# Kernel tuning notes

Measured on AMD Instinct MI355X. Metric: run time of the kernel, lower is better.

## Reference

```python
import jax, jax.numpy as jnp
import numpy as np
from jax import lax

N_BITS = 4  # init kwarg n_bits
Q_SCALE = 2.0 ** (N_BITS - 1) - 1.0  # signed n-bit levels


def ste_round(x):
    # straight-through rounding (identity gradient)
    return x + lax.stop_gradient(jnp.round(x) - x)


def quant_signed(x):
    # clip to [-1,1], quantize to 2^(n-1)-1 signed levels with STE
    return ste_round(jnp.clip(x, -1.0, 1.0) * Q_SCALE) / Q_SCALE


def qconv(x, w):
    # QuantizeConv: 3x3 stride-1 pad-1 conv with n-bit quantized weights
    return lax.conv_general_dilated(x, quant_signed(w), window_strides=(1, 1),
                                    padding=((1, 1), (1, 1)),
                                    dimension_numbers=('NCHW', 'OIHW', 'NCHW'))


def qact_conv(x, g, b):
    # QuantizeSignedActSBN (conv): per-channel scale/bias then signed quant
    return quant_signed(x * g[None, :, None, None] + b[None, :, None, None])


def qact_fc(x, g, b):
    return quant_signed(x * g[None, :] + b[None, :])


def maxpool2(x):
    return lax.reduce_window(x, -jnp.inf, lax.max, (1, 1, 2, 2), (1, 1, 2, 2), 'VALID')


def setup_inputs() -> dict:
    key = jax.random.key(0)
    ks = jax.random.split(key, 32)
    B = 512
    x = jax.random.normal(ks[0], (B, 3, 32, 32), dtype=jnp.float32)
    chans = [(64, 3), (64, 64), (128, 64), (128, 128), (256, 128), (256, 256)]
    inp = {'x': x}
    ki = 1
    for i, (co, ci) in enumerate(chans, start=1):
        inp[f'w{i}'] = jax.random.normal(ks[ki], (co, ci, 3, 3), dtype=jnp.float32) * 0.05; ki += 1
        inp[f'g{i}'] = jax.random.uniform(ks[ki], (co,), dtype=jnp.float32, minval=0.5, maxval=1.5); ki += 1
        inp[f'b{i}'] = jax.random.normal(ks[ki], (co,), dtype=jnp.float32) * 0.05; ki += 1
    # FC head: 4096 -> 512 -> 10 (torch Linear weight layout [out, in])
    inp['wf1'] = jax.random.normal(ks[ki], (512, 4096), dtype=jnp.float32) * 0.02; ki += 1
    inp['gf1'] = jax.random.uniform(ks[ki], (512,), dtype=jnp.float32, minval=0.5, maxval=1.5); ki += 1
    inp['bf1'] = jax.random.normal(ks[ki], (512,), dtype=jnp.float32) * 0.05; ki += 1
    inp['wf2'] = jax.random.normal(ks[ki], (10, 512), dtype=jnp.float32) * 0.05; ki += 1
    inp['gf2'] = jax.random.uniform(ks[ki], (10,), dtype=jnp.float32, minval=0.5, maxval=1.5); ki += 1
    inp['bf2'] = jax.random.normal(ks[ki], (10,), dtype=jnp.float32) * 0.05; ki += 1
    return inp


def reference(x, w1, g1, b1, w2, g2, b2, w3, g3, b3, w4, g4, b4, w5, g5, b5, w6, g6, b6,
              wf1, gf1, bf1, wf2, gf2, bf2):
    h = jax.nn.relu(qact_conv(qconv(x, w1), g1, b1))
    h = jax.nn.relu(qact_conv(qconv(h, w2), g2, b2))
    h = maxpool2(h)  # 32 -> 16
    h = jax.nn.relu(qact_conv(qconv(h, w3), g3, b3))
    h = jax.nn.relu(qact_conv(qconv(h, w4), g4, b4))
    h = maxpool2(h)  # 16 -> 8
    h = jax.nn.relu(qact_conv(qconv(h, w5), g5, b5))
    h = jax.nn.relu(qact_conv(qconv(h, w6), g6, b6))
    h = maxpool2(h)  # 8 -> 4 => 256*4*4 = 4096
    h = h.reshape(h.shape[0], -1)
    h = jax.nn.relu(qact_fc(h @ quant_signed(wf1).T, gf1, bf1))
    h = qact_fc(h @ quant_signed(wf2).T, gf2, bf2)
    return h
```

## Files before the change

### kernel.cpp

```cpp
#include <hip/hip_runtime.h>


typedef __attribute__((ext_vector_type(4))) int v4i;

#if defined(__has_builtin)
# if __has_builtin(__builtin_amdgcn_sdot4)
#  define HAS_SDOT4 1
# endif
#endif

__device__ __forceinline__ int dot4_i8(int a, int b, int c) {
#ifdef HAS_SDOT4
    return __builtin_amdgcn_sdot4(a, b, c, false);
#else
    c += ((a      ) & 0xff) * (int)(signed char)(b      );
    c += ((a >>  8) & 0xff) * (int)(signed char)(b >>  8);
    c += ((a >> 16) & 0xff) * (int)(signed char)(b >> 16);
    c += ((a >> 24) & 0xff) * (int)(signed char)(b >> 24);
    return c;
#endif
}

__device__ __forceinline__ void gld_lds16(const void* g, void* l) {
    __builtin_amdgcn_global_load_lds(
        (const __attribute__((address_space(1))) unsigned int*)g,
        (__attribute__((address_space(3))) unsigned int*)l, 16, 0, 0);
}

#define O_QW1    0u
#define O_QWF2   4096u
#define O_ZERO   10240u
#define O_QWT2   16384u
#define O_QWT3   65536u
#define O_QWT4   147456u
#define O_QWT5   294912u
#define O_QWT6   589824u
#define O_QWF1   1179648u
#define O_BUFA   3276800u
#define O_BUFB   36831232u

__device__ __forceinline__ signed char quant_w(double v) {
    return (signed char)(int)rint(fmin(fmax(v, -1.0), 1.0) * 7.0);
}

__device__ __forceinline__ void quantw_body(const float* __restrict__ w,
                                            signed char* __restrict__ q, int i, int n) {
    if (i < n) q[i] = quant_w((double)w[i]);
}

__device__ __forceinline__ void quantw_t8p_body(const float* __restrict__ w,
                                                signed char* __restrict__ o,
                                                int CI, int i, int n) {
    if (i < n) {
        const int b  = i & 15;
        const int t  = i >> 4;
        const int rows_per_grp = CI * 36;
        const int grp  = t / rows_per_grp;
        int rr = t - grp * rows_per_grp;
        const int pass = rr / 2304;
        rr -= pass * 2304;
        const int c    = rr / 576;
        const int row  = rr - c * 576;
        const int co_l = row / 9;
        const int tap  = row - co_l * 9;
        const int co = grp * 64 + co_l;
        const int ci = pass * 64 + c * 16 + b;
        o[i] = quant_w((double)w[(co * CI + ci) * 9 + tap]);
    }
}

__device__ __forceinline__ void quantw_fc1_body(const float* __restrict__ w,
                                                signed char* __restrict__ o, int i) {
    if (i < 512 * 4096) {
        int j  = i >> 12;
        int kn = i & 4095;
        int px = kn >> 8;
        int c  = kn & 255;
        int ko = c * 16 + px;
        o[i] = quant_w((double)w[j * 4096 + ko]);
    }
}

__global__ __launch_bounds__(256) void prep_k(
    const float* __restrict__ w1,  signed char* __restrict__ qw1,
    const float* __restrict__ wf2, signed char* __restrict__ qwf2,
    const float* __restrict__ w2,  signed char* __restrict__ qwt2,
    const float* __restrict__ w3,  signed char* __restrict__ qwt3,
    const float* __restrict__ w4,  signed char* __restrict__ qwt4,
    const float* __restrict__ w5,  signed char* __restrict__ qwt5,
    const float* __restrict__ w6,  signed char* __restrict__ qwt6,
    const float* __restrict__ wf1, signed char* __restrict__ qwf1,
    unsigned char* __restrict__ zs)
{
    const int blk = blockIdx.x;
    const int t   = threadIdx.x;
    if (blk == 0 && t < 16) ((int4*)zs)[t] = int4{0, 0, 0, 0};
    if      (blk < 7)    quantw_body(w1, qw1, blk * 256 + t, 1728);
    else if (blk < 27)   quantw_body(wf2, qwf2, (blk - 7) * 256 + t, 5120);
    else if (blk < 171)  quantw_t8p_body(w2, qwt2, 64,  (blk - 27)   * 256 + t, 36864);
    else if (blk < 459)  quantw_t8p_body(w3, qwt3, 64,  (blk - 171)  * 256 + t, 73728);
    else if (blk < 1035) quantw_t8p_body(w4, qwt4, 128, (blk - 459)  * 256 + t, 147456);
    else if (blk < 2187) quantw_t8p_body(w5, qwt5, 128, (blk - 1035) * 256 + t, 294912);
    else if (blk < 4491) quantw_t8p_body(w6, qwt6, 256, (blk - 2187) * 256 + t, 589824);
    else                 quantw_fc1_body(wf1, qwf1, (blk - 4491) * 256 + t);
}

#define XSTR 34
#define XPL  (10 * XSTR)
__global__ __launch_bounds__(256) void conv1_k(
    const float* __restrict__ x, const signed char* __restrict__ wq,
    const float* __restrict__ gvec, const float* __restrict__ bvec,
    unsigned char* __restrict__ out)
{
    __shared__ double xs[3 * XPL];
    __shared__ double wd[16 * 27];
    __shared__ __align__(16) unsigned char ob[256 * 16];

    const int tid  = threadIdx.x;
    const int sp   = tid & 63;
    const int cg   = tid >> 6;
    const int img  = blockIdx.x >> 2;
    const int slab = blockIdx.x & 3;
    const int y0s  = slab * 8;
    const int co_base = blockIdx.y * 16;
    const int yb = sp >> 4, xb = sp & 15;
    const int ysl = yb * 2, x0 = xb * 2;

    for (int i = tid; i < 432; i += 256)
        wd[i] = (double)wq[co_base * 27 + i];
    for (int i = tid; i < 3 * XPL; i += 256) {
        int ci = i / XPL, r = i - ci * XPL;
        int ry = r / XSTR, rx = r - ry * XSTR;
        int gy = y0s - 1 + ry, gx = rx - 1;
        double v = 0.0;
        if ((unsigned)gy < 32u && (unsigned)gx < 32u)
            v = (double)x[(img * 3 + ci) * 1024 + gy * 32 + gx];
        xs[i] = v;
    }
    __syncthreads();

    double acc[4][4];
#pragma unroll
    for (int l = 0; l < 4; ++l)
#pragma unroll
        for (int p = 0; p < 4; ++p) acc[l][p] = 0.0;

#pragma unroll
    for (int ci = 0; ci < 3; ++ci) {
        double a[4][4];
#pragma unroll
        for (int iy = 0; iy < 4; ++iy)
#pragma unroll
            for (int ix = 0; ix < 4; ++ix)
                a[iy][ix] = xs[ci * XPL + (ysl + iy) * XSTR + (x0 + ix)];
#pragma unroll
        for (int l = 0; l < 4; ++l) {
            const double* wr = &wd[((cg * 4 + l) * 3 + ci) * 9];
#pragma unroll
            for (int ky = 0; ky < 3; ++ky)
#pragma unroll
                for (int kx = 0; kx < 3; ++kx) {
                    const double wv = wr[ky * 3 + kx];
                    acc[l][0] = fma(wv, a[ky    ][kx    ], acc[l][0]);
                    acc[l][1] = fma(wv, a[ky    ][kx + 1], acc[l][1]);
                    acc[l][2] = fma(wv, a[ky + 1][kx    ], acc[l][2]);
                    acc[l][3] = fma(wv, a[ky + 1][kx + 1], acc[l][3]);
                }
        }
    }

    int qv[4][4];
#pragma unroll
    for (int l = 0; l < 4; ++l) {
        const int co = co_base + cg * 4 + l;
        const double gg  = (double)gvec[co];
        const double bb7 = (double)bvec[co] * 7.0;
#pragma unroll
        for (int p = 0; p < 4; ++p) {
            int qi = (int)rint(fma(acc[l][p], gg, bb7));
            qv[l][p] = qi < 0 ? 0 : (qi > 7 ? 7 : qi);
        }
    }
#pragma unroll
    for (int p = 0; p < 4; ++p) {
        unsigned int wv = (unsigned int)qv[0][p]
                        | ((unsigned int)qv[1][p] << 8)
                        | ((unsigned int)qv[2][p] << 16)
                        | ((unsigned int)qv[3][p] << 24);
        const int r = ysl + (p >> 1), c = x0 + (p & 1);
        const int px = r * 32 + c;
        const int slot = (cg ^ ((px >> 3) & 3) ^ ((px >> 6) & 3)) & 3;
        *(unsigned int*)&ob[px * 16 + slot * 4] = wv;
    }
    __syncthreads();
    {
        uint4 d = *(const uint4*)&ob[tid * 16];
        const int s = (((tid >> 3) & 3) ^ ((tid >> 6) & 3)) & 3;
        unsigned e0 = d.x, e1 = d.y, e2 = d.z, e3 = d.w, t;
        if (s & 1) { t = e0; e0 = e1; e1 = t; t = e2; e2 = e3; e3 = t; }
        if (s & 2) { t = e0; e0 = e2; e2 = t; t = e1; e1 = e3; e3 = t; }
        uint4 o; o.x = e0; o.y = e1; o.z = e2; o.w = e3;
        const int row = tid >> 5, col = tid & 31;
        *(uint4*)&out[((img * 32 + y0s + row) * 32 + col) * 64 + co_base] = o;
    }
}

template<int CI, int CO, int H, int W, bool POOL, int IPB>
__global__ __launch_bounds__(256, 2) void conv_i8_k(
    const unsigned char* __restrict__ in, const signed char* __restrict__ wt,
    const float* __restrict__ gvec, const float* __restrict__ bvec,
    unsigned char* __restrict__ out, const unsigned char* __restrict__ zs)
{
    constexpr int ATX    = (IPB == 1) ? 18 : 10;
    constexpr int APX    = ATX * ATX;
    constexpr int APLANE = IPB * APX * 16;
    constexpr int WBASE  = 4 * APLANE;
    constexpr int WPLANE = 576 * 16;
    constexpr int NPASS  = CI / 64;

    __shared__ __align__(16) char lds[WBASE + 4 * WPLANE];

    const int tid = threadIdx.x;
    const int l   = tid & 63;
    const int w   = tid >> 6;
    const int n   = l & 15;
    const int q   = l >> 4;

    int img = 0, regY0 = 0, regX0 = 0, wy8 = 0, wx8 = 0, tilepx = 0;
    if (IPB == 1) {
        constexpr int rpw = W / 16;
        constexpr int rpi = (H / 16) * rpw;
        img   = blockIdx.x / rpi;
        int r = blockIdx.x % rpi;
        regY0 = (r / rpw) * 16;
        regX0 = (r % rpw) * 16;
        wy8 = (w >> 1) * 8; wx8 = (w & 1) * 8;
    } else {
        tilepx = w * APX;
    }
    const int co_base = blockIdx.y * 64;

    const int ly = ((n >> 3) & 1) * 2 + ((n >> 1) & 1);
    const int lx = ((n >> 2) & 1) * 2 + (n & 1);

    int abase[4], wbase[4];
#pragma unroll
    for (int ps = 0; ps < 4; ++ps) {
        int ay0 = wy8 + (ps >> 1) * 4 + ly;
        int ax0 = wx8 + (ps & 1) * 4 + lx;
        abase[ps] = q * APLANE + (tilepx + ay0 * ATX + ax0) * 16;
    }
#pragma unroll
    for (int cs = 0; cs < 4; ++cs)
        wbase[cs] = WBASE + q * WPLANE + ((cs * 16 + n) * 9) * 16;

    v4i acc[4][4];
#pragma unroll
    for (int ps = 0; ps < 4; ++ps)
#pragma unroll
        for (int cs = 0; cs < 4; ++cs)
            acc[ps][cs] = (v4i)0;

    for (int pass = 0; pass < NPASS; ++pass) {
        const int cib = pass * 64;
        __syncthreads();
#pragma unroll
        for (int c = 0; c < 4; ++c) {
            for (int base = 0; base < IPB * APX; base += 256) {
                const int px_g = base + tid;
                if (px_g < IPB * APX) {
                    int tile = 0, px = px_g;
                    if (IPB == 4) { tile = px_g / APX; px = px_g - tile * APX; }
                    const int gy = regY0 - 1 + px / ATX;
                    const int gx = regX0 - 1 + px % ATX;
                    const int bimg = (IPB == 1) ? img : ((int)blockIdx.x * 4 + tile);
                    const void* src =
                        ((unsigned)gy < (unsigned)H && (unsigned)gx < (unsigned)W)
                        ? (const void*)&in[((bimg * H + gy) * W + gx) * CI + cib + c * 16]
                        : (const void*)zs;
                    gld_lds16(src, &lds[c * APLANE + px_g * 16]);
                }
            }
        }
        {
            const signed char* wsrc = wt + (size_t)(blockIdx.y * NPASS + pass) * (4 * WPLANE);
#pragma unroll
            for (int base = 0; base < 2304; base += 256) {
                const int i = base + tid;
                gld_lds16(wsrc + i * 16, &lds[WBASE + i * 16]);
            }
        }
        __syncthreads();

#pragma unroll
        for (int tap = 0; tap < 9; ++tap) {
            const int toff = ((tap / 3) * ATX + (tap % 3)) * 16;
            v4i bf[4], af[4];
#pragma unroll
            for (int cs = 0; cs < 4; ++cs)
                bf[cs] = *(const v4i*)&lds[wbase[cs] + tap * 16];
#pragma unroll
            for (int ps = 0; ps < 4; ++ps)
                af[ps] = *(const v4i*)&lds[abase[ps] + toff];
#pragma unroll
            for (int ps = 0; ps < 4; ++ps)
#pragma unroll
                for (int cs = 0; cs < 4; ++cs)
                    acc[ps][cs] = __builtin_amdgcn_mfma_i32_16x16x64_i8(
                        af[ps], bf[cs], acc[ps][cs], 0, 0, 0);
        }
    }

    const int bimg = (IPB == 1) ? img : ((int)blockIdx.x * 4 + w);
#pragma unroll
    for (int cs = 0; cs < 4; ++cs) {
        const int co = co_base + cs * 16 + n;
        const double g7 = (double)gvec[co] * (1.0 / 7.0);
        const double b7 = (double)bvec[co] * 7.0;
#pragma unroll
        for (int ps = 0; ps < 4; ++ps) {
            const int Yb = regY0 + wy8 + (ps >> 1) * 4 + (q >> 1) * 2;
            const int Xb = regX0 + wx8 + (ps & 1) * 4 + (q & 1) * 2;
            if (POOL) {
                int ms = max(max(acc[ps][cs][0], acc[ps][cs][1]),
                             max(acc[ps][cs][2], acc[ps][cs][3]));
                int qi = (int)rint(fma((double)ms, g7, b7));
                qi = qi < 0 ? 0 : (qi > 7 ? 7 : qi);
                out[((bimg * (H / 2) + (Yb >> 1)) * (W / 2) + (Xb >> 1)) * CO + co] = (unsigned char)qi;
            } else {
#pragma unroll
                for (int r = 0; r < 4; ++r) {
                    int qi = (int)rint(fma((double)acc[ps][cs][r], g7, b7));
                    qi = qi < 0 ? 0 : (qi > 7 ? 7 : qi);
                    const int Y = Yb + (r >> 1), X = Xb + (r & 1);
                    out[((bimg * H + Y) * W + X) * CO + co] = (unsigned char)qi;
                }
            }
        }
    }
}

__global__ __launch_bounds__(256, 2) void fc1_i8_k(
    const unsigned char* __restrict__ h, const signed char* __restrict__ wt,
    const float* __restrict__ gvec, const float* __restrict__ bvec,
    unsigned char* __restrict__ out)
{
    __shared__ int red[4096];
    const int tid = threadIdx.x;
    const int l = tid & 63, w = tid >> 6;
    const int n = l & 15, q = l >> 4;
    const int m0 = blockIdx.x * 32, n0 = blockIdx.y * 32;

    v4i acc[2][2];
#pragma unroll
    for (int a = 0; a < 2; ++a)
#pragma unroll
        for (int b = 0; b < 2; ++b) acc[a][b] = (v4i)0;

    const int kb = w * 1024;
    for (int ks = 0; ks < 16; ++ks) {
        const int k = kb + ks * 64 + q * 16;
        v4i af[2], bf[2];
#pragma unroll
        for (int ms = 0; ms < 2; ++ms)
            af[ms] = *(const v4i*)&h[(m0 + ms * 16 + n) * 4096 + k];
#pragma unroll
        for (int ns = 0; ns < 2; ++ns)
            bf[ns] = *(const v4i*)&wt[(n0 + ns * 16 + n) * 4096 + k];
#pragma unroll
        for (int ms = 0; ms < 2; ++ms)
#pragma unroll
            for (int ns = 0; ns < 2; ++ns)
                acc[ms][ns] = __builtin_amdgcn_mfma_i32_16x16x64_i8(
                    af[ms], bf[ns], acc[ms][ns], 0, 0, 0);
    }

#pragma unroll
    for (int ms = 0; ms < 2; ++ms)
#pragma unroll
        for (int ns = 0; ns < 2; ++ns)
#pragma unroll
            for (int r = 0; r < 4; ++r)
                red[w * 1024 + (ms * 16 + q * 4 + r) * 32 + ns * 16 + n] = acc[ms][ns][r];
    __syncthreads();

#pragma unroll
    for (int j = 0; j < 4; ++j) {
        const int e = tid * 4 + j;
        int s = red[e] + red[1024 + e] + red[2048 + e] + red[3072 + e];
        const int ml = e >> 5, nl = e & 31;
        const int co = n0 + nl;
        double y7 = fma((double)s, (double)gvec[co] * (1.0 / 7.0), (double)bvec[co] * 7.0);
        int qi = (int)rint(y7);
        qi = qi < 0 ? 0 : (qi > 7 ? 7 : qi);
        out[(m0 + ml) * 512 + co] = (unsigned char)qi;
    }
}

__global__ __launch_bounds__(256) void fc2_k(
    const unsigned char* __restrict__ h, const signed char* __restrict__ wq,
    const float* __restrict__ gvec, const float* __restrict__ bvec,
    float* __restrict__ out)
{
    const int gid = blockIdx.x * 256 + threadIdx.x;
    const int b = gid >> 4;
    const int n = gid & 15;
    if (b >= 512 || n >= 10) return;
    const int* hp = (const int*)&h[b * 512];
    const int* wp = (const int*)&wq[n * 512];
    int s = 0;
#pragma unroll 4
    for (int k = 0; k < 128; k += 4) {
        int4 hv = *(const int4*)&hp[k];
        int4 wv = *(const int4*)&wp[k];
        s = dot4_i8(hv.x, wv.x, s);
        s = dot4_i8(hv.y, wv.y, s);
        s = dot4_i8(hv.z, wv.z, s);
        s = dot4_i8(hv.w, wv.w, s);
    }
    double y7 = fma((double)s, (double)gvec[n] * (1.0 / 7.0), (double)bvec[n] * 7.0);
    double r = rint(y7);
    r = fmin(fmax(r, -7.0), 7.0);
    out[b * 10 + n] = (float)(r / 7.0);
}

extern "C" void kernel_launch(void* const* d_in, const int* in_sizes, int n_in,
                              void* d_out, int out_size, void* d_ws, size_t ws_size,
                              hipStream_t stream) {
    const float* x   = (const float*)d_in[0];
    const float* w1  = (const float*)d_in[1];
    const float* g1  = (const float*)d_in[2];
    const float* b1  = (const float*)d_in[3];
    const float* w2  = (const float*)d_in[4];
    const float* g2  = (const float*)d_in[5];
    const float* b2  = (const float*)d_in[6];
    const float* w3  = (const float*)d_in[7];
    const float* g3  = (const float*)d_in[8];
    const float* b3  = (const float*)d_in[9];
    const float* w4  = (const float*)d_in[10];
    const float* g4  = (const float*)d_in[11];
    const float* b4  = (const float*)d_in[12];
    const float* w5  = (const float*)d_in[13];
    const float* g5  = (const float*)d_in[14];
    const float* b5  = (const float*)d_in[15];
    const float* w6  = (const float*)d_in[16];
    const float* g6  = (const float*)d_in[17];
    const float* b6  = (const float*)d_in[18];
    const float* wf1 = (const float*)d_in[19];
    const float* gf1 = (const float*)d_in[20];
    const float* bf1 = (const float*)d_in[21];
    const float* wf2 = (const float*)d_in[22];
    const float* gf2 = (const float*)d_in[23];
    const float* bf2 = (const float*)d_in[24];

    char* ws = (char*)d_ws;
    signed char*   qw1  = (signed char*)(ws + O_QW1);
    signed char*   qwf2 = (signed char*)(ws + O_QWF2);
    unsigned char* zs   = (unsigned char*)(ws + O_ZERO);
    signed char*   qwt2 = (signed char*)(ws + O_QWT2);
    signed char*   qwt3 = (signed char*)(ws + O_QWT3);
    signed char*   qwt4 = (signed char*)(ws + O_QWT4);
    signed char*   qwt5 = (signed char*)(ws + O_QWT5);
    signed char*   qwt6 = (signed char*)(ws + O_QWT6);
    signed char*   qwf1 = (signed char*)(ws + O_QWF1);
    unsigned char* bufA = (unsigned char*)(ws + O_BUFA);
    unsigned char* bufB = (unsigned char*)(ws + O_BUFB);

    hipLaunchKernelGGL(prep_k, dim3(12683), dim3(256), 0, stream,
                       w1, qw1, wf2, qwf2, w2, qwt2, w3, qwt3,
                       w4, qwt4, w5, qwt5, w6, qwt6, wf1, qwf1, zs);

    hipLaunchKernelGGL(conv1_k, dim3(2048, 4), dim3(256), 0, stream, x, qw1, g1, b1, bufA);
    hipLaunchKernelGGL((conv_i8_k<64,  64,  32, 32, true,  1>), dim3(2048, 1), dim3(256), 0, stream, bufA, qwt2, g2, b2, bufB, zs);
    hipLaunchKernelGGL((conv_i8_k<64,  128, 16, 16, false, 1>), dim3(512,  2), dim3(256), 0, stream, bufB, qwt3, g3, b3, bufA, zs);
    hipLaunchKernelGGL((conv_i8_k<128, 128, 16, 16, true,  1>), dim3(512,  2), dim3(256), 0, stream, bufA, qwt4, g4, b4, bufB, zs);
    hipLaunchKernelGGL((conv_i8_k<128, 256, 8,  8,  false, 4>), dim3(128,  4), dim3(256), 0, stream, bufB, qwt5, g5, b5, bufA, zs);
    hipLaunchKernelGGL((conv_i8_k<256, 256, 8,  8,  true,  4>), dim3(128,  4), dim3(256), 0, stream, bufA, qwt6, g6, b6, bufB, zs);

    hipLaunchKernelGGL(fc1_i8_k, dim3(16, 16), dim3(256), 0, stream, bufB, qwf1, gf1, bf1, bufA);
    hipLaunchKernelGGL(fc2_k, dim3(32), dim3(256), 0, stream, bufA, qwf2, gf2, bf2, (float*)d_out);
}
```

Baseline: 269.4 us.

## Switch activations to channel-group planar layout and reuse weights across tiles

Activations move from NHWC to a layout of 16-channel groups, each stored as a contiguous pixel plane, so every 16-byte staging load reads consecutive pixels. The conv1 output store, the conv epilogues and the fc1 weight permutation are updated to match. The conv kernel also gains a TPB parameter, so a block with a single channel pass loads its weight slice into LDS once and loops over several spatial tiles, reducing repeated weight staging for conv2 and conv3. The cost is fewer blocks for those layers and scattered single-byte epilogue writes.

```diff
diff --git a/kernel.cpp b/kernel.cpp
--- a/kernel.cpp
+++ b/kernel.cpp
@@ -74,9 +74,11 @@
     if (i < 512 * 4096) {
         int j  = i >> 12;
         int kn = i & 4095;
-        int px = kn >> 8;
-        int c  = kn & 255;
-        int ko = c * 16 + px;
+        int gp = kn >> 8;
+        int r  = kn & 255;
+        int px = r >> 4;
+        int b  = r & 15;
+        int ko = (gp * 16 + b) * 16 + px;
         o[i] = quant_w((double)w[j * 4096 + ko]);
     }
 }
@@ -200,12 +202,12 @@
         if (s & 1) { t = e0; e0 = e1; e1 = t; t = e2; e2 = e3; e3 = t; }
         if (s & 2) { t = e0; e0 = e2; e2 = t; t = e1; e1 = e3; e3 = t; }
         uint4 o; o.x = e0; o.y = e1; o.z = e2; o.w = e3;
-        const int row = tid >> 5, col = tid & 31;
-        *(uint4*)&out[((img * 32 + y0s + row) * 32 + col) * 64 + co_base] = o;
-    }
-}
-
-template<int CI, int CO, int H, int W, bool POOL, int IPB>
+        *(uint4*)&out[(size_t)img * 65536 + (size_t)blockIdx.y * 16384
+                      + y0s * 512 + tid * 16] = o;
+    }
+}
+
+template<int CI, int CO, int H, int W, bool POOL, int IPB, int TPB>
 __global__ __launch_bounds__(256, 2) void conv_i8_k(
     const unsigned char* __restrict__ in, const signed char* __restrict__ wt,
     const float* __restrict__ gvec, const float* __restrict__ bvec,
@@ -217,6 +219,11 @@
     constexpr int WBASE  = 4 * APLANE;
     constexpr int WPLANE = 576 * 16;
     constexpr int NPASS  = CI / 64;
+    constexpr int PIN    = CI / 16;
+    constexpr int PXI    = H * W;
+    constexpr int POUT   = CO / 16;
+    constexpr int PXO    = POOL ? (H / 2) * (W / 2) : H * W;
+    static_assert(TPB == 1 || (NPASS == 1 && IPB == 1), "TPB>1 needs NPASS==1");
 
     __shared__ __align__(16) char lds[WBASE + 4 * WPLANE];
 
@@ -226,19 +233,10 @@
     const int n   = l & 15;
     const int q   = l >> 4;
 
-    int img = 0, regY0 = 0, regX0 = 0, wy8 = 0, wx8 = 0, tilepx = 0;
-    if (IPB == 1) {
-        constexpr int rpw = W / 16;
-        constexpr int rpi = (H / 16) * rpw;
-        img   = blockIdx.x / rpi;
-        int r = blockIdx.x % rpi;
-        regY0 = (r / rpw) * 16;
-        regX0 = (r % rpw) * 16;
-        wy8 = (w >> 1) * 8; wx8 = (w & 1) * 8;
-    } else {
-        tilepx = w * APX;
-    }
     const int co_base = blockIdx.y * 64;
+    const int wy8 = (IPB == 1) ? (w >> 1) * 8 : 0;
+    const int wx8 = (IPB == 1) ? (w & 1) * 8 : 0;
+    const int tilepx = (IPB == 4) ? w * APX : 0;
 
     const int ly = ((n >> 3) & 1) * 2 + ((n >> 1) & 1);
     const int lx = ((n >> 2) & 1) * 2 + (n & 1);
@@ -254,18 +252,10 @@
     for (int cs = 0; cs < 4; ++cs)
         wbase[cs] = WBASE + q * WPLANE + ((cs * 16 + n) * 9) * 16;
 
-    v4i acc[4][4];
-#pragma unroll
-    for (int ps = 0; ps < 4; ++ps)
-#pragma unroll
-        for (int cs = 0; cs < 4; ++cs)
-            acc[ps][cs] = (v4i)0;
-
-    for (int pass = 0; pass < NPASS; ++pass) {
-        const int cib = pass * 64;
-        __syncthreads();
+    auto stage_act = [&](int img0, int regY0, int regX0, int pass) {
 #pragma unroll
         for (int c = 0; c < 4; ++c) {
+            const int gp = pass * 4 + c;
             for (int base = 0; base < IPB * APX; base += 256) {
                 const int px_g = base + tid;
                 if (px_g < IPB * APX) {
@@ -273,25 +263,23 @@
                     if (IPB == 4) { tile = px_g / APX; px = px_g - tile * APX; }
                     const int gy = regY0 - 1 + px / ATX;
                     const int gx = regX0 - 1 + px % ATX;
-                    const int bimg = (IPB == 1) ? img : ((int)blockIdx.x * 4 + tile);
+                    const int bimg = img0 + tile;
                     const void* src =
                         ((unsigned)gy < (unsigned)H && (unsigned)gx < (unsigned)W)
-                        ? (const void*)&in[((bimg * H + gy) * W + gx) * CI + cib + c * 16]
+                        ? (const void*)&in[((size_t)(bimg * PIN + gp) * PXI + gy * W + gx) * 16]
                         : (const void*)zs;
                     gld_lds16(src, &lds[c * APLANE + px_g * 16]);
                 }
             }
         }
-        {
-            const signed char* wsrc = wt + (size_t)(blockIdx.y * NPASS + pass) * (4 * WPLANE);
-#pragma unroll
-            for (int base = 0; base < 2304; base += 256) {
-                const int i = base + tid;
-                gld_lds16(wsrc + i * 16, &lds[WBASE + i * 16]);
-            }
-        }
-        __syncthreads();
-
+    };
+    auto stage_w = [&](int pass) {
+        const signed char* wsrc = wt + (size_t)(blockIdx.y * NPASS + pass) * (4 * WPLANE);
+#pragma unroll
+        for (int base = 0; base < 2304; base += 256)
+            gld_lds16(wsrc + (base + tid) * 16, &lds[WBASE + (base + tid) * 16]);
+    };
+    auto taps = [&](v4i acc[4][4]) {
 #pragma unroll
         for (int tap = 0; tap < 9; ++tap) {
             const int toff = ((tap / 3) * ATX + (tap % 3)) * 16;
@@ -309,33 +297,88 @@
                     acc[ps][cs] = __builtin_amdgcn_mfma_i32_16x16x64_i8(
                         af[ps], bf[cs], acc[ps][cs], 0, 0, 0);
         }
-    }
-
-    const int bimg = (IPB == 1) ? img : ((int)blockIdx.x * 4 + w);
-#pragma unroll
-    for (int cs = 0; cs < 4; ++cs) {
-        const int co = co_base + cs * 16 + n;
-        const double g7 = (double)gvec[co] * (1.0 / 7.0);
-        const double b7 = (double)bvec[co] * 7.0;
-#pragma unroll
-        for (int ps = 0; ps < 4; ++ps) {
-            const int Yb = regY0 + wy8 + (ps >> 1) * 4 + (q >> 1) * 2;
-            const int Xb = regX0 + wx8 + (ps & 1) * 4 + (q & 1) * 2;
-            if (POOL) {
-                int ms = max(max(acc[ps][cs][0], acc[ps][cs][1]),
-                             max(acc[ps][cs][2], acc[ps][cs][3]));
-                int qi = (int)rint(fma((double)ms, g7, b7));
-                qi = qi < 0 ? 0 : (qi > 7 ? 7 : qi);
-                out[((bimg * (H / 2) + (Yb >> 1)) * (W / 2) + (Xb >> 1)) * CO + co] = (unsigned char)qi;
-            } else {
-#pragma unroll
-                for (int r = 0; r < 4; ++r) {
-                    int qi = (int)rint(fma((double)acc[ps][cs][r], g7, b7));
+    };
+    auto epilogue = [&](v4i acc[4][4], int img0, int regY0, int regX0) {
+        const int bimg = (IPB == 1) ? img0 : (img0 + w);
+#pragma unroll
+        for (int cs = 0; cs < 4; ++cs) {
+            const int co = co_base + cs * 16 + n;
+            const int pl = (co_base >> 4) + cs;
+            const double g7 = (double)gvec[co] * (1.0 / 7.0);
+            const double b7 = (double)bvec[co] * 7.0;
+#pragma unroll
+            for (int ps = 0; ps < 4; ++ps) {
+                const int Yb = regY0 + wy8 + (ps >> 1) * 4 + (q >> 1) * 2;
+                const int Xb = regX0 + wx8 + (ps & 1) * 4 + (q & 1) * 2;
+                if (POOL) {
+                    int ms = max(max(acc[ps][cs][0], acc[ps][cs][1]),
+                                 max(acc[ps][cs][2], acc[ps][cs][3]));
+                    int qi = (int)rint(fma((double)ms, g7, b7));
                     qi = qi < 0 ? 0 : (qi > 7 ? 7 : qi);
-                    const int Y = Yb + (r >> 1), X = Xb + (r & 1);
-                    out[((bimg * H + Y) * W + X) * CO + co] = (unsigned char)qi;
+                    out[((size_t)(bimg * POUT + pl) * PXO + (Yb >> 1) * (W / 2) + (Xb >> 1)) * 16 + n]
+                        = (unsigned char)qi;
+                } else {
+#pragma unroll
+                    for (int r = 0; r < 4; ++r) {
+                        int qi = (int)rint(fma((double)acc[ps][cs][r], g7, b7));
+                        qi = qi < 0 ? 0 : (qi > 7 ? 7 : qi);
+                        const int Y = Yb + (r >> 1), X = Xb + (r & 1);
+                        out[((size_t)(bimg * POUT + pl) * PXO + Y * W + X) * 16 + n]
+                            = (unsigned char)qi;
+                    }
                 }
             }
+        }
+    };
+
+    if (TPB == 1) {
+        int img = 0, regY0 = 0, regX0 = 0;
+        if (IPB == 1) {
+            constexpr int rpw = W / 16;
+            constexpr int rpi = (H / 16) * rpw;
+            img   = blockIdx.x / rpi;
+            int r = blockIdx.x % rpi;
+            regY0 = (r / rpw) * 16;
+            regX0 = (r % rpw) * 16;
+        } else {
+            img = (int)blockIdx.x * 4;
+        }
+        v4i acc[4][4];
+#pragma unroll
+        for (int ps = 0; ps < 4; ++ps)
+#pragma unroll
+            for (int cs = 0; cs < 4; ++cs) acc[ps][cs] = (v4i)0;
+
+        for (int pass = 0; pass < NPASS; ++pass) {
+            __syncthreads();
+            stage_act(img, regY0, regX0, pass);
+            stage_w(pass);
+            __syncthreads();
+            taps(acc);
+        }
+        epilogue(acc, img, regY0, regX0);
+    } else {
+        stage_w(0);
+        for (int tt = 0; tt < TPB; ++tt) {
+            const int t = (int)blockIdx.x * TPB + tt;
+            int img, regY0 = 0, regX0 = 0;
+            if (H == 32) {
+                img = t >> 2;
+                regY0 = ((t >> 1) & 1) * 16;
+                regX0 = (t & 1) * 16;
+            } else {
+                img = t;
+            }
+            __syncthreads();
+            stage_act(img, regY0, regX0, 0);
+            __syncthreads();
+            v4i acc[4][4];
+#pragma unroll
+            for (int ps = 0; ps < 4; ++ps)
+#pragma unroll
+                for (int cs = 0; cs < 4; ++cs) acc[ps][cs] = (v4i)0;
+            taps(acc);
+            epilogue(acc, img, regY0, regX0);
         }
     }
 }
@@ -471,11 +514,11 @@
                        w4, qwt4, w5, qwt5, w6, qwt6, wf1, qwf1, zs);
 
     hipLaunchKernelGGL(conv1_k, dim3(2048, 4), dim3(256), 0, stream, x, qw1, g1, b1, bufA);
-    hipLaunchKernelGGL((conv_i8_k<64,  64,  32, 32, true,  1>), dim3(2048, 1), dim3(256), 0, stream, bufA, qwt2, g2, b2, bufB, zs);
-    hipLaunchKernelGGL((conv_i8_k<64,  128, 16, 16, false, 1>), dim3(512,  2), dim3(256), 0, stream, bufB, qwt3, g3, b3, bufA, zs);
-    hipLaunchKernelGGL((conv_i8_k<128, 128, 16, 16, true,  1>), dim3(512,  2), dim3(256), 0, stream, bufA, qwt4, g4, b4, bufB, zs);
-    hipLaunchKernelGGL((conv_i8_k<128, 256, 8,  8,  false, 4>), dim3(128,  4), dim3(256), 0, stream, bufB, qwt5, g5, b5, bufA, zs);
-    hipLaunchKernelGGL((conv_i8_k<256, 256, 8,  8,  true,  4>), dim3(128,  4), dim3(256), 0, stream, bufA, qwt6, g6, b6, bufB, zs);
+    hipLaunchKernelGGL((conv_i8_k<64,  64,  32, 32, true,  1, 4>), dim3(512,  1), dim3(256), 0, stream, bufA, qwt2, g2, b2, bufB, zs);
+    hipLaunchKernelGGL((conv_i8_k<64,  128, 16, 16, false, 1, 2>), dim3(256,  2), dim3(256), 0, stream, bufB, qwt3, g3, b3, bufA, zs);
+    hipLaunchKernelGGL((conv_i8_k<128, 128, 16, 16, true,  1, 1>), dim3(512,  2), dim3(256), 0, stream, bufA, qwt4, g4, b4, bufB, zs);
+    hipLaunchKernelGGL((conv_i8_k<128, 256, 8,  8,  false, 4, 1>), dim3(128,  4), dim3(256), 0, stream, bufB, qwt5, g5, b5, bufA, zs);
+    hipLaunchKernelGGL((conv_i8_k<256, 256, 8,  8,  true,  4, 1>), dim3(128,  4), dim3(256), 0, stream, bufA, qwt6, g6, b6, bufB, zs);
 
     hipLaunchKernelGGL(fc1_i8_k, dim3(16, 16), dim3(256), 0, stream, bufB, qwf1, gf1, bf1, bufA);
     hipLaunchKernelGGL(fc2_k, dim3(32), dim3(256), 0, stream, bufA, qwf2, gf2, bf2, (float*)d_out);
```

Result: faster. 254.2 us (-5.7%).
